# Kernel optimization log

Measured on AMD Instinct MI355X. Metric: run time of the kernel, lower is better.

## Reference

```python
import jax, jax.numpy as jnp
import numpy as np

N_NODES = 100000
N_EDGES = 1600000
HEADS = 8
CH = 16
NEG_SLOPE = 0.2


def setup_inputs() -> dict:
    key = jax.random.key(0)
    ks = jax.random.split(key, 8)
    x = jax.random.normal(ks[0], (N_NODES, 16), dtype=jnp.float32)
    edge_index = jax.random.randint(ks[1], (2, N_EDGES), 0, N_NODES, dtype=jnp.int64)
    W = jax.random.normal(ks[2], (16, HEADS * CH), dtype=jnp.float32) * 0.25
    att_src = jax.random.normal(ks[3], (HEADS, CH), dtype=jnp.float32) * 0.25
    att_dst = jax.random.normal(ks[4], (HEADS, CH), dtype=jnp.float32) * 0.25
    bias = jax.random.normal(ks[5], (HEADS * CH,), dtype=jnp.float32) * 0.1
    fc_w = jax.random.normal(ks[6], (HEADS * CH, 5), dtype=jnp.float32) * 0.1
    fc_b = jax.random.normal(ks[7], (5,), dtype=jnp.float32) * 0.1
    return {"x": x, "edge_index": edge_index, "W": W, "att_src": att_src,
            "att_dst": att_dst, "bias": bias, "fc_w": fc_w, "fc_b": fc_b}


def reference(x, edge_index, W, att_src, att_dst, bias, fc_w, fc_b):
    N = x.shape[0]
    # PyG GATConv default: add self loops
    loops = jnp.arange(N, dtype=edge_index.dtype)
    src = jnp.concatenate([edge_index[0], loops])
    dst = jnp.concatenate([edge_index[1], loops])

    h = (x @ W).reshape(N, HEADS, CH)                 # [N,H,C]
    a_src = jnp.einsum('nhc,hc->nh', h, att_src)      # [N,H]
    a_dst = jnp.einsum('nhc,hc->nh', h, att_dst)      # [N,H]

    e = a_src[src] + a_dst[dst]                       # [E,H]
    e = jax.nn.leaky_relu(e, NEG_SLOPE)
    # segment softmax over edges grouped by destination node
    e_max = jax.ops.segment_max(e, dst, num_segments=N)
    e_exp = jnp.exp(e - e_max[dst])
    denom = jax.ops.segment_sum(e_exp, dst, num_segments=N)
    alpha = e_exp / (denom[dst] + 1e-16)              # [E,H]

    msg = alpha[:, :, None] * h[src]                  # [E,H,C]
    out = jax.ops.segment_sum(msg, dst, num_segments=N)  # [N,H,C]
    out = out.reshape(N, HEADS * CH) + bias           # concat heads + bias

    out = jax.nn.relu(out)
    # dropout is identity in eval mode
    logits = out @ fc_w + fc_b                        # [N,5]
    return jax.nn.log_softmax(logits, axis=1)
```

## Files before the change

kernel.cpp:

```cpp
#include <hip/hip_runtime.h>
#include <hip/hip_bf16.h>
#include <hip/hip_fp16.h>
#include <math.h>

#define N_NODES 100000
#define N_EDGES 1600000
#define HEADS 8
#define HC 128
#define LOG2E 1.44269504f

#define DPB 64
#define NB 1563
#define NBP (NB + 1)
#define NCH 512
#define EPC (N_EDGES / NCH)
#define CAPS 1664
#define WSTR (CAPS + 4)
#define NA 196

__global__ __launch_bounds__(512) void k_prep(
    const float* __restrict__ x, const float* __restrict__ W,
    const float* __restrict__ att_s, const float* __restrict__ att_d,
    const int* __restrict__ ei,
    unsigned short* __restrict__ a_srcb, float* __restrict__ a_dst,
    uint4* __restrict__ x2b,
    int* __restrict__ offs, unsigned* __restrict__ stg) {
    __shared__ int smem[2048 + EPC];
    __shared__ int ws8[8];
    int t = threadIdx.x;
    if (blockIdx.x >= NCH) {
        float* sM = (float*)smem;
        if (t < 256) {
            int k = t >> 4, h2 = t & 15;
            const float* av = (h2 < 8) ? att_s : att_d;
            int h = h2 & 7;
            float s = 0.f;
#pragma unroll
            for (int c = 0; c < 16; ++c)
                s = fmaf(W[k * HC + h * 16 + c], av[h * 16 + c], s);
            sM[k * 16 + h2] = s * LOG2E;
        }
        __syncthreads();
        int node = (blockIdx.x - NCH) * 512 + t;
        if (node < N_NODES) {
            const float4* xr = (const float4*)(x + node * 16);
            float4 x0 = xr[0], x1 = xr[1], x2 = xr[2], x3 = xr[3];
            float xv[16] = {x0.x, x0.y, x0.z, x0.w, x1.x, x1.y, x1.z, x1.w,
                            x2.x, x2.y, x2.z, x2.w, x3.x, x3.y, x3.z, x3.w};
            union { uint4 u[2]; __hip_bfloat162 b[8]; } px;
#pragma unroll
            for (int k = 0; k < 8; ++k)
                px.b[k] = __float22bfloat162_rn(float2{xv[2 * k], xv[2 * k + 1]});
            x2b[node * 2] = px.u[0];
            x2b[node * 2 + 1] = px.u[1];
            float oo[16];
#pragma unroll
            for (int h2 = 0; h2 < 16; ++h2) {
                float o = 0.f;
#pragma unroll
                for (int k = 0; k < 16; ++k) o = fmaf(xv[k], sM[k * 16 + h2], o);
                oo[h2] = o;
            }
            union { uint4 u; unsigned short s[8]; } pb;
#pragma unroll
            for (int h = 0; h < 8; ++h)
                pb.s[h] = __bfloat16_as_ushort(__float2bfloat16(oo[h]));
            *(uint4*)(a_srcb + (size_t)node * 8) = pb.u;
            float4 d0 = {oo[8], oo[9], oo[10], oo[11]};
            float4 d1 = {oo[12], oo[13], oo[14], oo[15]};
            *(float4*)(a_dst + (size_t)node * 8) = d0;
            *(float4*)(a_dst + (size_t)node * 8 + 4) = d1;
        }
    } else {
        int* hist = smem;
        unsigned* entries = (unsigned*)(smem + 2048);
        int c = blockIdx.x;
        hist[t] = 0; hist[t + 512] = 0; hist[t + 1024] = 0; hist[t + 1536] = 0;
        __syncthreads();
        int beg = c * EPC, end = beg + EPC;
        for (int e = beg + t; e < end; e += 512)
            atomicAdd(&hist[ei[N_EDGES + e] >> 6], 1);
        __syncthreads();
        int i0 = 4 * t;
        int v0 = hist[i0], v1 = hist[i0 + 1], v2 = hist[i0 + 2], v3 = hist[i0 + 3];
        int s1 = v0 + v1, s2 = s1 + v2, T = s2 + v3;
        int lane = t & 63, wv = t >> 6;
        int inc = T;
#pragma unroll
        for (int off = 1; off < 64; off <<= 1) {
            int y = __shfl_up(inc, off);
            if (lane >= off) inc += y;
        }
        if (lane == 63) ws8[wv] = inc;
        __syncthreads();
        int wbase = 0;
        for (int k = 0; k < wv; ++k) wbase += ws8[k];
        int e0 = wbase + inc - T;
        hist[i0] = e0; hist[i0 + 1] = e0 + v0;
        hist[i0 + 2] = e0 + s1; hist[i0 + 3] = e0 + s2;
        __syncthreads();
        int row = c * NBP;
        for (int b = t; b < NB; b += 512) offs[row + b] = hist[b];
        if (t == 0) offs[row + NB] = EPC;
        __syncthreads();
        for (int e = beg + t; e < end; e += 512) {
            int src = ei[e], dst = ei[N_EDGES + e];
            int pos = atomicAdd(&hist[dst >> 6], 1);
            entries[pos] = ((unsigned)(dst & 63) << 17) | (unsigned)src;
        }
        __syncthreads();
        unsigned* so = stg + beg;
        for (int i = t; i < EPC; i += 512) so[i] = entries[i];
    }
}

__global__ __launch_bounds__(512) void k_gather(
    const __hip_bfloat162* __restrict__ x2b,
    const unsigned short* __restrict__ a_srcb, const float* __restrict__ W,
    const float* __restrict__ a_dst,
    const int* __restrict__ offs, const unsigned* __restrict__ stg,
    const float* __restrict__ bias, const float* __restrict__ fc_w,
    const float* __restrict__ fc_b, float* __restrict__ out) {
    __shared__ __align__(16) unsigned buf0[(8 * WSTR) / 2];
    __shared__ __align__(16) int sbuf[CAPS];
    __shared__ __align__(16) float sW[16 * HC];
    __shared__ __align__(16) float sad[8 * DPB + 8];
    __shared__ int hist[DPB];
    __shared__ int bs[DPB + 1];
    __shared__ int ws8[8];
    unsigned* estage = buf0;
    unsigned short* wst = (unsigned short*)buf0;
    int* cstage = sbuf;
    int* o0_s = sbuf;
    int* myb_s = sbuf + 512;
    int b = blockIdx.x, t = threadIdx.x;
    int d0 = b * DPB;
    for (int i = t; i < 16 * HC; i += 512) {
        int c = i & 127, k = i >> 7;
        int blk = c >> 3;
        int sb = blk ^ ((blk >> 2) & 3);
        sW[k * HC + sb * 8 + (c & 7)] = W[i];
    }
    sad[t] = (d0 * 8 + t < N_NODES * 8) ? a_dst[(size_t)d0 * 8 + t] : 0.f;
    if (t < 8) sad[8 * DPB + t] = -100000.f;
    int lane = t & 63, wv = t >> 6;
    {
        int o0 = offs[t * NBP + b];
        int len = offs[t * NBP + b + 1] - o0;
        o0_s[t] = o0;
        int inc = len;
#pragma unroll
        for (int off = 1; off < 64; off <<= 1) {
            int y = __shfl_up(inc, off);
            if (lane >= off) inc += y;
        }
        if (lane == 63) ws8[wv] = inc;
        __syncthreads();
        int wbase = 0;
        for (int k = 0; k < wv; ++k) wbase += ws8[k];
        myb_s[t] = wbase + inc - len;
        if (t == 511) myb_s[NCH] = wbase + inc;
    }
    if (t < DPB) hist[t] = (d0 + t < N_NODES) ? 1 : 0;
    __syncthreads();
    int tot = myb_s[NCH];
    for (int i = t; i < tot; i += 512) {
        int lo = 0, hi = NCH - 1;
#pragma unroll
        for (int s = 0; s < 9; ++s) {
            int mid = (lo + hi + 1) >> 1;
            if (myb_s[mid] <= i) lo = mid; else hi = mid - 1;
        }
        unsigned u = stg[lo * EPC + o0_s[lo] + (i - myb_s[lo])];
        estage[i] = u;
        atomicAdd(&hist[u >> 17], 1);
    }
    __syncthreads();
    if (t < 64) {
        int gd = d0 + t;
        bool val = gd < N_NODES;
        int len = hist[t];
        int plen = (len + 3) & ~3;
        int iv = plen;
#pragma unroll
        for (int off = 1; off < 64; off <<= 1) {
            int y = __shfl_up(iv, off);
            if (t >= off) iv += y;
        }
        int excl = iv - plen;
        bs[t] = excl;
        if (t == 63) bs[64] = iv;
        if (val) cstage[excl] = (t << 17) | gd;
        hist[t] = excl + (val ? 1 : 0);
        for (int k = len; k < plen; ++k) cstage[excl + k] = (64 << 17);
    }
    __syncthreads();
    for (int i = t; i < tot; i += 512) {
        unsigned u = estage[i];
        int pos = atomicAdd(&hist[u >> 17], 1);
        cstage[pos] = (int)u;
    }
    __syncthreads();
    int ctot = bs[DPB];
    for (int i = t; i < ctot; i += 512) {
        unsigned u = (unsigned)cstage[i];
        int s = (int)(u & 0x1FFFF);
        int dl = (int)(u >> 17);
        union { uint4 v; __hip_bfloat162 b2[4]; } pa;
        pa.v = *(const uint4*)(a_srcb + (size_t)s * 8);
        const float* adp = sad + dl * 8;
        float4 ad0 = *(const float4*)(adp);
        float4 ad1 = *(const float4*)(adp + 4);
        float2 s01 = __bfloat1622float2(pa.b2[0]);
        float2 s23 = __bfloat1622float2(pa.b2[1]);
        float2 s45 = __bfloat1622float2(pa.b2[2]);
        float2 s67 = __bfloat1622float2(pa.b2[3]);
        float e[8] = {s01.x + ad0.x, s01.y + ad0.y, s23.x + ad0.z, s23.y + ad0.w,
                      s45.x + ad1.x, s45.y + ad1.y, s67.x + ad1.z, s67.y + ad1.w};
#pragma unroll
        for (int h = 0; h < 8; ++h) {
            float eh = fmaxf(e[h], 0.2f * e[h]);
            float w = exp2f(eh);
            wst[h * WSTR + i] = __half_as_ushort(__float2half(w));
        }
    }
    __syncthreads();
    int q = t & 15, g = t >> 4;
    int head = q >> 1, i8 = q & 1;
    int c0 = head * 16 + i8 * 8;
    int blk0 = c0 >> 3;
    int sw0 = (blk0 ^ ((blk0 >> 2) & 3)) * 8;
    const unsigned short* wrow = wst + head * WSTR;
    int xofs = i8 * 16;
    const char* xb = (const char*)x2b;
    float bb[8], fwv[8][5], fbv[5];
#pragma unroll
    for (int m = 0; m < 8; ++m) bb[m] = bias[c0 + m];
#pragma unroll
    for (int m = 0; m < 8; ++m)
#pragma unroll
        for (int jj = 0; jj < 5; ++jj) fwv[m][jj] = fc_w[(c0 + m) * 5 + jj];
#pragma unroll
    for (int jj = 0; jj < 5; ++jj) fbv[jj] = fc_b[jj];
    for (int l4 = 0; l4 < 2; ++l4) {
        int l = g * 2 + l4;
        int gd = d0 + l;
        if (gd >= N_NODES) break;
        int beg = bs[l], end = bs[l + 1];
        float A[8] = {0.f, 0.f, 0.f, 0.f, 0.f, 0.f, 0.f, 0.f};
        float wsum = 0.f;
        auto acc = [&](const uint4& xv, float w) {
            union { uint4 v; __hip_bfloat162 b2[4]; } xx; xx.v = xv;
            float2 f0 = __bfloat1622float2(xx.b2[0]);
            float2 f1 = __bfloat1622float2(xx.b2[1]);
            float2 f2 = __bfloat1622float2(xx.b2[2]);
            float2 f3 = __bfloat1622float2(xx.b2[3]);
            A[0] = fmaf(w, f0.x, A[0]); A[1] = fmaf(w, f0.y, A[1]);
            A[2] = fmaf(w, f1.x, A[2]); A[3] = fmaf(w, f1.y, A[3]);
            A[4] = fmaf(w, f2.x, A[4]); A[5] = fmaf(w, f2.y, A[5]);
            A[6] = fmaf(w, f3.x, A[6]); A[7] = fmaf(w, f3.y, A[7]);
        };
        for (int j = beg; j < end; j += 4) {
            int4 cs = *(const int4*)(cstage + j);
            uint2 wu = *(const uint2*)(wrow + j);
            union { uint2 u2; __half2 h2[2]; } wq; wq.u2 = wu;
            float2 w01 = __half22float2(wq.h2[0]);
            float2 w23 = __half22float2(wq.h2[1]);
            int s0 = cs.x & 0x1FFFF, s1 = cs.y & 0x1FFFF;
            int s2 = cs.z & 0x1FFFF, s3 = cs.w & 0x1FFFF;
            uint4 xv0 = *(const uint4*)(xb + ((s0 << 5) + xofs));
            uint4 xv1 = *(const uint4*)(xb + ((s1 << 5) + xofs));
            uint4 xv2 = *(const uint4*)(xb + ((s2 << 5) + xofs));
            uint4 xv3 = *(const uint4*)(xb + ((s3 << 5) + xofs));
            acc(xv0, w01.x); acc(xv1, w01.y);
            acc(xv2, w23.x); acc(xv3, w23.y);
            wsum += (w01.x + w01.y) + (w23.x + w23.y);
        }
        float inv = 1.f / (wsum + 1e-16f);
#pragma unroll
        for (int m = 0; m < 8; ++m) A[m] *= inv;
        float ov[8] = {0.f, 0.f, 0.f, 0.f, 0.f, 0.f, 0.f, 0.f};
#pragma unroll
        for (int m = 0; m < 8; ++m) {
            float a = A[m];
            float ap = __shfl_xor(A[m], 1);
            const float* w0r = sW + (i8 * 8 + m) * HC + sw0;
            const float* w1r = sW + ((1 - i8) * 8 + m) * HC + sw0;
#pragma unroll
            for (int o = 0; o < 8; ++o) ov[o] = fmaf(a, w0r[o], ov[o]);
#pragma unroll
            for (int o = 0; o < 8; ++o) ov[o] = fmaf(ap, w1r[o], ov[o]);
        }
#pragma unroll
        for (int m = 0; m < 8; ++m) ov[m] = fmaxf(ov[m] + bb[m], 0.f);
        float p[5];
#pragma unroll
        for (int jj = 0; jj < 5; ++jj) {
            float sacc = 0.f;
#pragma unroll
            for (int m = 0; m < 8; ++m) sacc = fmaf(ov[m], fwv[m][jj], sacc);
            p[jj] = sacc;
        }
#pragma unroll
        for (int off = 8; off >= 1; off >>= 1)
#pragma unroll
            for (int jj = 0; jj < 5; ++jj) p[jj] += __shfl_xor(p[jj], off);
        if (q == 0) {
            float lg[5], mx = -1e30f;
#pragma unroll
            for (int jj = 0; jj < 5; ++jj) {
                lg[jj] = p[jj] + fbv[jj];
                mx = fmaxf(mx, lg[jj]);
            }
            float sum = 0.f;
#pragma unroll
            for (int jj = 0; jj < 5; ++jj) sum += __expf(lg[jj] - mx);
            float ls = mx + __logf(sum);
#pragma unroll
            for (int jj = 0; jj < 5; ++jj) out[gd * 5 + jj] = lg[jj] - ls;
        }
    }
}

extern "C" void kernel_launch(void* const* d_in, const int* in_sizes, int n_in,
                              void* d_out, int out_size, void* d_ws, size_t ws_size,
                              hipStream_t stream) {
    const float* x     = (const float*)d_in[0];
    const int*   ei    = (const int*)d_in[1];
    const float* W     = (const float*)d_in[2];
    const float* att_s = (const float*)d_in[3];
    const float* att_d = (const float*)d_in[4];
    const float* bias  = (const float*)d_in[5];
    const float* fc_w  = (const float*)d_in[6];
    const float* fc_b  = (const float*)d_in[7];
    float* out = (float*)d_out;

    char* ws = (char*)d_ws;
    size_t off = 0;
    auto carve = [&](size_t bytes) {
        void* p = ws + off;
        off = (off + bytes + 255) & ~(size_t)255;
        return p;
    };
    unsigned short* a_srcb = (unsigned short*)carve((size_t)N_NODES * HEADS * 2);
    float*    a_dst = (float*)   carve((size_t)N_NODES * HEADS * 4);
    uint4*    x2b   = (uint4*)   carve((size_t)N_NODES * 32);
    int*      offs  = (int*)     carve((size_t)NCH * NBP * 4);
    unsigned* stg   = (unsigned*)carve((size_t)N_EDGES * 4);

    k_prep<<<NCH + NA, 512, 0, stream>>>(x, W, att_s, att_d, ei,
                                         a_srcb, a_dst, x2b, offs, stg);
    k_gather<<<NB, 512, 0, stream>>>((const __hip_bfloat162*)x2b, a_srcb, W,
                                     a_dst, offs, stg, bias, fc_w, fc_b, out);
}
```

Baseline: 162.4 us.

## Pack per-node attention and features into one record; fuse weight calc into scatter

```diff
diff --git a/kernel.cpp b/kernel.cpp
--- a/kernel.cpp
+++ b/kernel.cpp
@@ -17,13 +17,13 @@
 #define CAPS 1664
 #define WSTR (CAPS + 4)
 #define NA 196
+#define NRB 48
 
 __global__ __launch_bounds__(512) void k_prep(
     const float* __restrict__ x, const float* __restrict__ W,
     const float* __restrict__ att_s, const float* __restrict__ att_d,
     const int* __restrict__ ei,
-    unsigned short* __restrict__ a_srcb, float* __restrict__ a_dst,
-    uint4* __restrict__ x2b,
+    char* __restrict__ nrec, float* __restrict__ a_dst,
     int* __restrict__ offs, unsigned* __restrict__ stg) {
     __shared__ int smem[2048 + EPC];
     __shared__ int ws8[8];
@@ -51,8 +51,6 @@
 #pragma unroll
             for (int k = 0; k < 8; ++k)
                 px.b[k] = __float22bfloat162_rn(float2{xv[2 * k], xv[2 * k + 1]});
-            x2b[node * 2] = px.u[0];
-            x2b[node * 2 + 1] = px.u[1];
             float oo[16];
 #pragma unroll
             for (int h2 = 0; h2 < 16; ++h2) {
@@ -65,7 +63,10 @@
 #pragma unroll
             for (int h = 0; h < 8; ++h)
                 pb.s[h] = __bfloat16_as_ushort(__float2bfloat16(oo[h]));
-            *(uint4*)(a_srcb + (size_t)node * 8) = pb.u;
+            char* r = nrec + (size_t)node * NRB;
+            *(uint4*)r = pb.u;
+            *(uint4*)(r + 16) = px.u[0];
+            *(uint4*)(r + 32) = px.u[1];
             float4 d0 = {oo[8], oo[9], oo[10], oo[11]};
             float4 d1 = {oo[12], oo[13], oo[14], oo[15]};
             *(float4*)(a_dst + (size_t)node * 8) = d0;
@@ -115,21 +116,19 @@
 }
 
 __global__ __launch_bounds__(512) void k_gather(
-    const __hip_bfloat162* __restrict__ x2b,
-    const unsigned short* __restrict__ a_srcb, const float* __restrict__ W,
+    const char* __restrict__ nrec, const float* __restrict__ W,
     const float* __restrict__ a_dst,
     const int* __restrict__ offs, const unsigned* __restrict__ stg,
     const float* __restrict__ bias, const float* __restrict__ fc_w,
     const float* __restrict__ fc_b, float* __restrict__ out) {
-    __shared__ __align__(16) unsigned buf0[(8 * WSTR) / 2];
+    __shared__ __align__(16) unsigned short wst[8 * WSTR];
+    __shared__ __align__(16) unsigned estg[CAPS];
     __shared__ __align__(16) int sbuf[CAPS];
     __shared__ __align__(16) float sW[16 * HC];
-    __shared__ __align__(16) float sad[8 * DPB + 8];
+    __shared__ __align__(16) float sad[8 * DPB];
     __shared__ int hist[DPB];
     __shared__ int bs[DPB + 1];
     __shared__ int ws8[8];
-    unsigned* estage = buf0;
-    unsigned short* wst = (unsigned short*)buf0;
     int* cstage = sbuf;
     int* o0_s = sbuf;
     int* myb_s = sbuf + 512;
@@ -142,7 +141,6 @@
         sW[k * HC + sb * 8 + (c & 7)] = W[i];
     }
     sad[t] = (d0 * 8 + t < N_NODES * 8) ? a_dst[(size_t)d0 * 8 + t] : 0.f;
-    if (t < 8) sad[8 * DPB + t] = -100000.f;
     int lane = t & 63, wv = t >> 6;
     {
         int o0 = offs[t * NBP + b];
@@ -172,7 +170,7 @@
             if (myb_s[mid] <= i) lo = mid; else hi = mid - 1;
         }
         unsigned u = stg[lo * EPC + o0_s[lo] + (i - myb_s[lo])];
-        estage[i] = u;
+        estg[i] = u;
         atomicAdd(&hist[u >> 17], 1);
     }
     __syncthreads();
@@ -190,24 +188,43 @@
         int excl = iv - plen;
         bs[t] = excl;
         if (t == 63) bs[64] = iv;
-        if (val) cstage[excl] = (t << 17) | gd;
         hist[t] = excl + (val ? 1 : 0);
-        for (int k = len; k < plen; ++k) cstage[excl + k] = (64 << 17);
+        for (int k = len; k < plen; ++k) {
+            cstage[excl + k] = 0;
+#pragma unroll
+            for (int h = 0; h < 8; ++h) wst[h * WSTR + excl + k] = 0;
+        }
+        if (val) {
+            cstage[excl] = (t << 17) | gd;
+            union { uint4 v; __hip_bfloat162 b2[4]; } pa;
+            pa.v = *(const uint4*)(nrec + (size_t)gd * NRB);
+            const float* adp = sad + t * 8;
+            float4 ad0 = *(const float4*)(adp);
+            float4 ad1 = *(const float4*)(adp + 4);
+            float2 s01 = __bfloat1622float2(pa.b2[0]);
+            float2 s23 = __bfloat1622float2(pa.b2[1]);
+            float2 s45 = __bfloat1622float2(pa.b2[2]);
+            float2 s67 = __bfloat1622float2(pa.b2[3]);
+            float e[8] = {s01.x + ad0.x, s01.y + ad0.y, s23.x + ad0.z,
+                          s23.y + ad0.w, s45.x + ad1.x, s45.y + ad1.y,
+                          s67.x + ad1.z, s67.y + ad1.w};
+#pragma unroll
+            for (int h = 0; h < 8; ++h) {
+                float eh = fmaxf(e[h], 0.2f * e[h]);
+                wst[h * WSTR + excl] =
+                    __half_as_ushort(__float2half(exp2f(eh)));
+            }
+        }
     }
     __syncthreads();
     for (int i = t; i < tot; i += 512) {
-        unsigned u = estage[i];
+        unsigned u = estg[i];
         int pos = atomicAdd(&hist[u >> 17], 1);
         cstage[pos] = (int)u;
-    }
-    __syncthreads();
-    int ctot = bs[DPB];
-    for (int i = t; i < ctot; i += 512) {
-        unsigned u = (unsigned)cstage[i];
         int s = (int)(u & 0x1FFFF);
         int dl = (int)(u >> 17);
         union { uint4 v; __hip_bfloat162 b2[4]; } pa;
-        pa.v = *(const uint4*)(a_srcb + (size_t)s * 8);
+        pa.v = *(const uint4*)(nrec + (size_t)s * NRB);
         const float* adp = sad + dl * 8;
         float4 ad0 = *(const float4*)(adp);
         float4 ad1 = *(const float4*)(adp + 4);
@@ -220,8 +237,7 @@
 #pragma unroll
         for (int h = 0; h < 8; ++h) {
             float eh = fmaxf(e[h], 0.2f * e[h]);
-            float w = exp2f(eh);
-            wst[h * WSTR + i] = __half_as_ushort(__float2half(w));
+            wst[h * WSTR + pos] = __half_as_ushort(__float2half(exp2f(eh)));
         }
     }
     __syncthreads();
@@ -231,8 +247,7 @@
     int blk0 = c0 >> 3;
     int sw0 = (blk0 ^ ((blk0 >> 2) & 3)) * 8;
     const unsigned short* wrow = wst + head * WSTR;
-    int xofs = i8 * 16;
-    const char* xb = (const char*)x2b;
+    int xofs = 16 + i8 * 16;
     float bb[8], fwv[8][5], fbv[5];
 #pragma unroll
     for (int m = 0; m < 8; ++m) bb[m] = bias[c0 + m];
@@ -268,10 +283,10 @@
             float2 w23 = __half22float2(wq.h2[1]);
             int s0 = cs.x & 0x1FFFF, s1 = cs.y & 0x1FFFF;
             int s2 = cs.z & 0x1FFFF, s3 = cs.w & 0x1FFFF;
-            uint4 xv0 = *(const uint4*)(xb + ((s0 << 5) + xofs));
-            uint4 xv1 = *(const uint4*)(xb + ((s1 << 5) + xofs));
-            uint4 xv2 = *(const uint4*)(xb + ((s2 << 5) + xofs));
-            uint4 xv3 = *(const uint4*)(xb + ((s3 << 5) + xofs));
+            uint4 xv0 = *(const uint4*)(nrec + s0 * NRB + xofs);
+            uint4 xv1 = *(const uint4*)(nrec + s1 * NRB + xofs);
+            uint4 xv2 = *(const uint4*)(nrec + s2 * NRB + xofs);
+            uint4 xv3 = *(const uint4*)(nrec + s3 * NRB + xofs);
             acc(xv0, w01.x); acc(xv1, w01.y);
             acc(xv2, w23.x); acc(xv3, w23.y);
             wsum += (w01.x + w01.y) + (w23.x + w23.y);
@@ -342,14 +357,13 @@
         off = (off + bytes + 255) & ~(size_t)255;
         return p;
     };
-    unsigned short* a_srcb = (unsigned short*)carve((size_t)N_NODES * HEADS * 2);
+    char*     nrec  = (char*)    carve((size_t)N_NODES * NRB);
     float*    a_dst = (float*)   carve((size_t)N_NODES * HEADS * 4);
-    uint4*    x2b   = (uint4*)   carve((size_t)N_NODES * 32);
     int*      offs  = (int*)     carve((size_t)NCH * NBP * 4);
     unsigned* stg   = (unsigned*)carve((size_t)N_EDGES * 4);
 
     k_prep<<<NCH + NA, 512, 0, stream>>>(x, W, att_s, att_d, ei,
-                                         a_srcb, a_dst, x2b, offs, stg);
-    k_gather<<<NB, 512, 0, stream>>>((const __hip_bfloat162*)x2b, a_srcb, W,
-                                     a_dst, offs, stg, bias, fc_w, fc_b, out);
+                                         nrec, a_dst, offs, stg);
+    k_gather<<<NB, 512, 0, stream>>>(nrec, W, a_dst, offs, stg,
+                                     bias, fc_w, fc_b, out);
 }
```

Measured after the change: 164.3 us. No clear change (+1.2%).
